# Kernel optimization log

Measured on AMD Instinct MI355X. Metric: run time of the kernel, lower is better.

Reference implementation:

```python
import jax, jax.numpy as jnp
import numpy as np

IN_DIM = 32
OUT_DIM = 32
VAR_DIM = 64
BATCH = 16384
KER_DIMS = [1024, 1024, 1024, 1024]
NUM_STEPS = 8  # fixed-step RK4 stand-in for adaptive odeint (tol=1e-4)


def setup_inputs() -> dict:
    key = jax.random.key(0)
    ks = jax.random.split(key, 12)
    x = jax.random.normal(ks[0], (BATCH, IN_DIM), dtype=jnp.float32)
    aug = jnp.ones((BATCH, VAR_DIM - IN_DIM), dtype=jnp.float32)
    dims = [VAR_DIM] + KER_DIMS + [VAR_DIM]
    inp = {"x": x, "aug": aug}
    for i, (d1, d2) in enumerate(zip(dims[:-1], dims[1:])):
        # Linear(d1+1, d2): weight (d2, d1+1), bias (d2,)
        inp[f"W{i}"] = jax.random.normal(ks[1 + 2 * i], (d2, d1 + 1), dtype=jnp.float32) * 0.02
        inp[f"b{i}"] = jax.random.normal(ks[2 + 2 * i], (d2,), dtype=jnp.float32) * 0.02
    return inp


def _odefunc(t, y, Ws, bs):
    # y: [B, VAR_DIM]; per-layer concat of scalar time column, Linear, ReLU (except last)
    out = y
    n = len(Ws)
    for i, (W, b) in enumerate(zip(Ws, bs)):
        z = jnp.concatenate([out, jnp.full((out.shape[0], 1), t, dtype=out.dtype)], axis=1)
        out = z @ W.T + b
        if i < n - 1:
            out = jax.nn.relu(out)
    return out


def _integrate(y0, Ws, bs):
    dt = jnp.float32(1.0 / NUM_STEPS)

    def rk4_step(y, t):
        k1 = _odefunc(t, y, Ws, bs)
        k2 = _odefunc(t + 0.5 * dt, y + 0.5 * dt * k1, Ws, bs)
        k3 = _odefunc(t + 0.5 * dt, y + 0.5 * dt * k2, Ws, bs)
        k4 = _odefunc(t + dt, y + dt * k3, Ws, bs)
        return y + (dt / 6.0) * (k1 + 2.0 * k2 + 2.0 * k3 + k4), None

    ts = jnp.arange(NUM_STEPS, dtype=jnp.float32) * dt
    y1, _ = jax.lax.scan(rk4_step, y0, ts)
    return y1


def reference(x, aug, W0, b0, W1, b1, W2, b2, W3, b3, W4, b4):
    Ws = (W0, W1, W2, W3, W4)
    bs = (b0, b1, b2, b3, b4)
    y0 = jnp.concatenate([x, aug], axis=1)  # [B, VAR_DIM]
    y1 = _integrate(y0, Ws, bs)
    return y1[:, :OUT_DIM]
```

## Files before the change

kernel.cpp:

```cpp
#include <hip/hip_runtime.h>
#include <cstdint>
#include <cstddef>

#define BATCH 16384

typedef float f32x4 __attribute__((ext_vector_type(4)));
typedef _Float16 f16x8 __attribute__((ext_vector_type(8)));

__device__ __forceinline__ unsigned short f2h_bits(float f) {
  _Float16 h = (_Float16)f;
  return __builtin_bit_cast(unsigned short, h);
}

__device__ __forceinline__ void async_cp16(const void* g, void* l) {
  __builtin_amdgcn_global_load_lds(
      (const __attribute__((address_space(1))) unsigned int*)g,
      (__attribute__((address_space(3))) unsigned int*)l, 16, 0, 0);
}

template <int BM, int BN, int RT, int CT, int K, int N, bool RELU>
__launch_bounds__(256, 2)
__global__ void gemm_h(const unsigned short* __restrict__ A,
                       const unsigned short* __restrict__ Bw,
                       const float* __restrict__ Wfull,
                       const float* __restrict__ bias,
                       float tval,
                       unsigned short* __restrict__ Ch) {
  constexpr int BK = 32;
  constexpr int NI = K / BK;
  __shared__ __align__(16) unsigned short smA[2][BM * BK];
  __shared__ __align__(16) unsigned short smB[2][BN * BK];
  __shared__ float biasLds[BN];

  const int tid = threadIdx.x;
  const int wave = tid >> 6;
  const int lane = tid & 63;
  const int quad = lane >> 4;
  const int r16 = lane & 15;

  const int rowA0 = blockIdx.x * BM;
  const int rowB0 = blockIdx.y * BN;
  const int waveM = wave >> 1;
  const int waveN = wave & 1;

  if (tid < BN) {
    const int col = rowB0 + tid;
    biasLds[tid] = bias[col] + tval * Wfull[(size_t)col * (K + 1) + K];
  }

  auto stage = [&](int k0, int buf) {
#pragma unroll
    for (int i = 0; i < BM * 4 / 256; ++i) {
      const int s = i * 256 + tid;
      const int row = s >> 2;
      const int c = (s & 3) ^ ((row >> 1) & 3);
      const unsigned short* g = A + (size_t)(rowA0 + row) * K + (k0 + c * 8);
      char* l = ((char*)smA[buf]) + (size_t)(i * 256 + (wave << 6)) * 16;
      async_cp16(g, l);
    }
#pragma unroll
    for (int i = 0; i < BN * 4 / 256; ++i) {
      const int s = i * 256 + tid;
      const int row = s >> 2;
      const int c = (s & 3) ^ ((row >> 1) & 3);
      const unsigned short* g = Bw + (size_t)(rowB0 + row) * K + (k0 + c * 8);
      char* l = ((char*)smB[buf]) + (size_t)(i * 256 + (wave << 6)) * 16;
      async_cp16(g, l);
    }
  };

  f32x4 acc[RT][CT];
  const f32x4 zero = {0.f, 0.f, 0.f, 0.f};
#pragma unroll
  for (int i = 0; i < RT; ++i)
#pragma unroll
    for (int j = 0; j < CT; ++j) acc[i][j] = zero;

  stage(0, 0);

#pragma unroll 2
  for (int kk = 0; kk < NI; ++kk) {
    __syncthreads();
    if (kk + 1 < NI) stage((kk + 1) * BK, (kk + 1) & 1);

    const unsigned short* sA = smA[kk & 1];
    const unsigned short* sB = smB[kk & 1];
    f16x8 af[RT], bfr[CT];
#pragma unroll
    for (int nt = 0; nt < CT; ++nt) {
      const int row = (waveN * CT + nt) * 16 + r16;
      const int cp = quad ^ ((row >> 1) & 3);
      bfr[nt] = *(const f16x8*)(sB + row * BK + cp * 8);
    }
#pragma unroll
    for (int mt = 0; mt < RT; ++mt) {
      const int row = (waveM * RT + mt) * 16 + r16;
      const int cp = quad ^ ((row >> 1) & 3);
      af[mt] = *(const f16x8*)(sA + row * BK + cp * 8);
    }
#pragma unroll
    for (int mt = 0; mt < RT; ++mt)
#pragma unroll
      for (int nt = 0; nt < CT; ++nt)
        acc[mt][nt] =
            __builtin_amdgcn_mfma_f32_16x16x32_f16(af[mt], bfr[nt], acc[mt][nt], 0, 0, 0);
  }

#pragma unroll
  for (int mt = 0; mt < RT; ++mt) {
    const int grow0 = rowA0 + (waveM * RT + mt) * 16 + quad * 4;
#pragma unroll
    for (int nt = 0; nt < CT; ++nt) {
      const int lcol = (waveN * CT + nt) * 16 + r16;
      const int gcol = rowB0 + lcol;
      const float bi = biasLds[lcol];
#pragma unroll
      for (int r = 0; r < 4; ++r) {
        float v = acc[mt][nt][r] + bi;
        if (RELU) v = fmaxf(v, 0.0f);
        Ch[(size_t)(grow0 + r) * N + gcol] = f2h_bits(v);
      }
    }
  }
}

__launch_bounds__(256, 4)
__global__ void gemm_l4(const unsigned short* __restrict__ A,
                        const unsigned short* __restrict__ Bw,
                        const float* __restrict__ Wfull,
                        const float* __restrict__ bias,
                        float tval,
                        float* __restrict__ y, float* __restrict__ ksum,
                        unsigned short* __restrict__ yh,
                        float* __restrict__ outp, int mode, float dt) {
  constexpr int K = 1024, BK = 32, BM = 32, BN = 64, NI = K / BK;
  __shared__ __align__(16) unsigned short smA[2][BM * BK];
  __shared__ __align__(16) unsigned short smB[2][BN * BK];
  __shared__ float biasLds[BN];

  const int tid = threadIdx.x;
  const int wave = tid >> 6;
  const int lane = tid & 63;
  const int quad = lane >> 4;
  const int r16 = lane & 15;

  const int rowA0 = blockIdx.x * BM;
  const int waveM = wave >> 1;
  const int waveN = wave & 1;

  if (tid < BN) {
    biasLds[tid] = bias[tid] + tval * Wfull[(size_t)tid * (K + 1) + K];
  }

  auto stage = [&](int k0, int buf) {
    if (tid < BM * 4) {
      const int s = tid;
      const int row = s >> 2;
      const int c = (s & 3) ^ ((row >> 1) & 3);
      const unsigned short* g = A + (size_t)(rowA0 + row) * K + (k0 + c * 8);
      char* l = ((char*)smA[buf]) + (size_t)(wave << 6) * 16;
      async_cp16(g, l);
    }
    {
      const int s = tid;
      const int row = s >> 2;
      const int c = (s & 3) ^ ((row >> 1) & 3);
      const unsigned short* g = Bw + (size_t)row * K + (k0 + c * 8);
      char* l = ((char*)smB[buf]) + (size_t)(wave << 6) * 16;
      async_cp16(g, l);
    }
  };

  f32x4 acc[2];
  const f32x4 zero = {0.f, 0.f, 0.f, 0.f};
  acc[0] = zero; acc[1] = zero;

  stage(0, 0);

#pragma unroll 2
  for (int kk = 0; kk < NI; ++kk) {
    __syncthreads();
    if (kk + 1 < NI) stage((kk + 1) * BK, (kk + 1) & 1);

    const unsigned short* sA = smA[kk & 1];
    const unsigned short* sB = smB[kk & 1];
    f16x8 af, bfr[2];
    {
      const int row = waveM * 16 + r16;
      const int cp = quad ^ ((row >> 1) & 3);
      af = *(const f16x8*)(sA + row * BK + cp * 8);
    }
#pragma unroll
    for (int nt = 0; nt < 2; ++nt) {
      const int row = (waveN * 2 + nt) * 16 + r16;
      const int cp = quad ^ ((row >> 1) & 3);
      bfr[nt] = *(const f16x8*)(sB + row * BK + cp * 8);
    }
#pragma unroll
    for (int nt = 0; nt < 2; ++nt)
      acc[nt] = __builtin_amdgcn_mfma_f32_16x16x32_f16(af, bfr[nt], acc[nt], 0, 0, 0);
  }

  const int grow0 = rowA0 + waveM * 16 + quad * 4;
#pragma unroll
  for (int nt = 0; nt < 2; ++nt) {
    const int col = waveN * 32 + nt * 16 + r16;
    const float bi = biasLds[col];
#pragma unroll
    for (int r = 0; r < 4; ++r) {
      const float k = acc[nt][r] + bi;
      const int row = grow0 + r;
      const int idx = row * 64 + col;
      if (mode == 0) {
        ksum[idx] = k;
        yh[idx] = f2h_bits(y[idx] + 0.5f * dt * k);
      } else if (mode == 1) {
        ksum[idx] += 2.f * k;
        yh[idx] = f2h_bits(y[idx] + 0.5f * dt * k);
      } else if (mode == 2) {
        ksum[idx] += 2.f * k;
        yh[idx] = f2h_bits(y[idx] + dt * k);
      } else {
        const float yn = y[idx] + (dt / 6.f) * (ksum[idx] + k);
        y[idx] = yn;
        yh[idx] = f2h_bits(yn);
        if (outp && col < 32) outp[row * 32 + col] = yn;
      }
    }
  }
}

__global__ void conv_w(const float* __restrict__ W, unsigned short* __restrict__ Wh,
                       int N, int K) {
  const int idx = blockIdx.x * 256 + threadIdx.x;
  if (idx < N * K) {
    const int n = idx / K;
    const int k = idx - n * K;
    Wh[idx] = f2h_bits(W[(size_t)n * (K + 1) + k]);
  }
}

__global__ void init_y(const float* __restrict__ x, const float* __restrict__ aug,
                       float* __restrict__ y, unsigned short* __restrict__ yh) {
  const int idx = blockIdx.x * 256 + threadIdx.x;
  const int i = idx >> 6;
  const int j = idx & 63;
  const float v = (j < 32) ? x[i * 32 + j] : aug[i * 32 + (j - 32)];
  y[idx] = v;
  yh[idx] = f2h_bits(v);
}

extern "C" void kernel_launch(void* const* d_in, const int* in_sizes, int n_in,
                              void* d_out, int out_size, void* d_ws, size_t ws_size,
                              hipStream_t stream) {
  const float* x = (const float*)d_in[0];
  const float* aug = (const float*)d_in[1];
  const float* W[5];
  const float* b[5];
  for (int i = 0; i < 5; ++i) {
    W[i] = (const float*)d_in[2 + 2 * i];
    b[i] = (const float*)d_in[3 + 2 * i];
  }

  char* ws = (char*)d_ws;
  auto alloc = [&](size_t bytes) -> char* {
    char* p = ws;
    ws += (bytes + 255) & ~(size_t)255;
    return p;
  };
  float* y = (float*)alloc((size_t)BATCH * 64 * 4);
  unsigned short* yh = (unsigned short*)alloc((size_t)BATCH * 64 * 2);
  unsigned short* h1 = (unsigned short*)alloc((size_t)BATCH * 1024 * 2);
  unsigned short* h2 = (unsigned short*)alloc((size_t)BATCH * 1024 * 2);
  float* ksum = (float*)alloc((size_t)BATCH * 64 * 4);
  const int Kdim[5] = {64, 1024, 1024, 1024, 1024};
  const int Ndim[5] = {1024, 1024, 1024, 1024, 64};
  unsigned short* Wh[5];
  for (int i = 0; i < 5; ++i)
    Wh[i] = (unsigned short*)alloc((size_t)Ndim[i] * Kdim[i] * 2);

  for (int i = 0; i < 5; ++i) {
    const int total = Ndim[i] * Kdim[i];
    conv_w<<<(total + 255) / 256, 256, 0, stream>>>(W[i], Wh[i], Ndim[i], Kdim[i]);
  }
  init_y<<<BATCH * 64 / 256, 256, 0, stream>>>(x, aug, y, yh);

  const float dt = 0.125f;
  float* outp = (float*)d_out;

  auto eval = [&](float t, int mode, float* op) {
    gemm_h<256, 128, 8, 4, 64, 1024, true>
        <<<dim3(BATCH / 256, 1024 / 128), 256, 0, stream>>>(
            yh, Wh[0], W[0], b[0], t, h1);
    unsigned short* src = h1;
    unsigned short* dst = h2;
    for (int L = 1; L <= 3; ++L) {
      gemm_h<256, 128, 8, 4, 1024, 1024, true>
          <<<dim3(BATCH / 256, 1024 / 128), 256, 0, stream>>>(
              src, Wh[L], W[L], b[L], t, dst);
      unsigned short* tmp = src; src = dst; dst = tmp;
    }
    gemm_l4<<<dim3(BATCH / 32, 1), 256, 0, stream>>>(
        src, Wh[4], W[4], b[4], t, y, ksum, yh, op, mode, dt);
  };

  for (int s = 0; s < 8; ++s) {
    const float t0 = s * dt;
    eval(t0, 0, nullptr);
    eval(t0 + 0.5f * dt, 1, nullptr);
    eval(t0 + 0.5f * dt, 2, nullptr);
    eval(t0 + dt, 3, (s == 7) ? outp : nullptr);
  }
}
```

Baseline: 4.855 ms.

## Pre-tile activations and weights into MFMA fragment layout, load fragments directly from global

Stores weights, activations and the y state in a 16-row tiled layout that matches the MFMA fragment order. Each wave can then load its A/B fragments straight from global memory into registers with register double-buffering, and the LDS staging and per-iteration barriers go away. Epilogues write through an LDS tile so the tiled output is stored as coalesced 16-byte chunks. The trade-offs are the loss of LDS-based reuse across waves, since each wave now reads the B tiles itself and leans on L2, and higher register pressure from full unrolling.

```diff
diff --git a/kernel.cpp b/kernel.cpp
--- a/kernel.cpp
+++ b/kernel.cpp
@@ -12,24 +12,18 @@
   return __builtin_bit_cast(unsigned short, h);
 }
 
-__device__ __forceinline__ void async_cp16(const void* g, void* l) {
-  __builtin_amdgcn_global_load_lds(
-      (const __attribute__((address_space(1))) unsigned int*)g,
-      (__attribute__((address_space(3))) unsigned int*)l, 16, 0, 0);
-}
-
-template <int BM, int BN, int RT, int CT, int K, int N, bool RELU>
+
+template <int RT, int CT, int K, bool RELU>
 __launch_bounds__(256, 2)
 __global__ void gemm_h(const unsigned short* __restrict__ A,
                        const unsigned short* __restrict__ Bw,
                        const float* __restrict__ Wfull,
                        const float* __restrict__ bias,
                        float tval,
-                       unsigned short* __restrict__ Ch) {
-  constexpr int BK = 32;
-  constexpr int NI = K / BK;
-  __shared__ __align__(16) unsigned short smA[2][BM * BK];
-  __shared__ __align__(16) unsigned short smB[2][BN * BK];
+                       unsigned short* __restrict__ Co) {
+  constexpr int NI = K / 32;
+  constexpr int BN = CT * 16;
+  __shared__ unsigned short ctile[256 * 136];
   __shared__ float biasLds[BN];
 
   const int tid = threadIdx.x;
@@ -38,36 +32,22 @@
   const int quad = lane >> 4;
   const int r16 = lane & 15;
 
-  const int rowA0 = blockIdx.x * BM;
+  const int rowA0 = blockIdx.x * 256;
   const int rowB0 = blockIdx.y * BN;
-  const int waveM = wave >> 1;
-  const int waveN = wave & 1;
 
   if (tid < BN) {
     const int col = rowB0 + tid;
     biasLds[tid] = bias[col] + tval * Wfull[(size_t)col * (K + 1) + K];
   }
 
-  auto stage = [&](int k0, int buf) {
-#pragma unroll
-    for (int i = 0; i < BM * 4 / 256; ++i) {
-      const int s = i * 256 + tid;
-      const int row = s >> 2;
-      const int c = (s & 3) ^ ((row >> 1) & 3);
-      const unsigned short* g = A + (size_t)(rowA0 + row) * K + (k0 + c * 8);
-      char* l = ((char*)smA[buf]) + (size_t)(i * 256 + (wave << 6)) * 16;
-      async_cp16(g, l);
-    }
-#pragma unroll
-    for (int i = 0; i < BN * 4 / 256; ++i) {
-      const int s = i * 256 + tid;
-      const int row = s >> 2;
-      const int c = (s & 3) ^ ((row >> 1) & 3);
-      const unsigned short* g = Bw + (size_t)(rowB0 + row) * K + (k0 + c * 8);
-      char* l = ((char*)smB[buf]) + (size_t)(i * 256 + (wave << 6)) * 16;
-      async_cp16(g, l);
-    }
-  };
+  const unsigned short* aptr[RT];
+#pragma unroll
+  for (int mt = 0; mt < RT; ++mt)
+    aptr[mt] = A + (size_t)(rowA0 / 16 + wave * RT + mt) * (K * 16) + lane * 8;
+  const unsigned short* bptr[CT];
+#pragma unroll
+  for (int nt = 0; nt < CT; ++nt)
+    bptr[nt] = Bw + (size_t)(rowB0 / 16 + nt) * (K * 16) + lane * 8;
 
   f32x4 acc[RT][CT];
   const f32x4 zero = {0.f, 0.f, 0.f, 0.f};
@@ -76,55 +56,61 @@
 #pragma unroll
     for (int j = 0; j < CT; ++j) acc[i][j] = zero;
 
-  stage(0, 0);
-
-#pragma unroll 2
+  f16x8 af[2][RT], bf[2][CT];
+  auto loadfr = [&](int kk, int s) {
+#pragma unroll
+    for (int mt = 0; mt < RT; ++mt)
+      af[s][mt] = *(const f16x8*)(aptr[mt] + (size_t)kk * 512);
+#pragma unroll
+    for (int nt = 0; nt < CT; ++nt)
+      bf[s][nt] = *(const f16x8*)(bptr[nt] + (size_t)kk * 512);
+  };
+
+  loadfr(0, 0);
+#pragma unroll
   for (int kk = 0; kk < NI; ++kk) {
-    __syncthreads();
-    if (kk + 1 < NI) stage((kk + 1) * BK, (kk + 1) & 1);
-
-    const unsigned short* sA = smA[kk & 1];
-    const unsigned short* sB = smB[kk & 1];
-    f16x8 af[RT], bfr[CT];
+    const int cur = kk & 1;
+    if (kk + 1 < NI) loadfr(kk + 1, cur ^ 1);
+#pragma unroll
+    for (int mt = 0; mt < RT; ++mt)
+#pragma unroll
+      for (int nt = 0; nt < CT; ++nt)
+        acc[mt][nt] = __builtin_amdgcn_mfma_f32_16x16x32_f16(
+            af[cur][mt], bf[cur][nt], acc[mt][nt], 0, 0, 0);
+  }
+
+  __syncthreads();
+
+#pragma unroll
+  for (int mt = 0; mt < RT; ++mt) {
+    const int row0 = wave * (RT * 16) + mt * 16 + quad * 4;
 #pragma unroll
     for (int nt = 0; nt < CT; ++nt) {
-      const int row = (waveN * CT + nt) * 16 + r16;
-      const int cp = quad ^ ((row >> 1) & 3);
-      bfr[nt] = *(const f16x8*)(sB + row * BK + cp * 8);
-    }
-#pragma unroll
-    for (int mt = 0; mt < RT; ++mt) {
-      const int row = (waveM * RT + mt) * 16 + r16;
-      const int cp = quad ^ ((row >> 1) & 3);
-      af[mt] = *(const f16x8*)(sA + row * BK + cp * 8);
-    }
-#pragma unroll
-    for (int mt = 0; mt < RT; ++mt)
-#pragma unroll
-      for (int nt = 0; nt < CT; ++nt)
-        acc[mt][nt] =
-            __builtin_amdgcn_mfma_f32_16x16x32_f16(af[mt], bfr[nt], acc[mt][nt], 0, 0, 0);
-  }
-
-#pragma unroll
-  for (int mt = 0; mt < RT; ++mt) {
-    const int grow0 = rowA0 + (waveM * RT + mt) * 16 + quad * 4;
-#pragma unroll
-    for (int nt = 0; nt < CT; ++nt) {
-      const int lcol = (waveN * CT + nt) * 16 + r16;
-      const int gcol = rowB0 + lcol;
-      const float bi = biasLds[lcol];
+      const int col = nt * 16 + r16;
+      const float bi = biasLds[col];
 #pragma unroll
       for (int r = 0; r < 4; ++r) {
         float v = acc[mt][nt][r] + bi;
         if (RELU) v = fmaxf(v, 0.0f);
-        Ch[(size_t)(grow0 + r) * N + gcol] = f2h_bits(v);
+        ctile[(row0 + r) * 136 + col] = f2h_bits(v);
       }
     }
   }
-}
-
-__launch_bounds__(256, 4)
+  __syncthreads();
+
+#pragma unroll
+  for (int i = 0; i < 16; ++i) {
+    const int chunk = i * 256 + tid;
+    const int r = chunk & 15;
+    const int kc = (chunk >> 4) & 15;
+    const int mt2 = chunk >> 8;
+    f16x8 vv = *(const f16x8*)(ctile + (mt2 * 16 + r) * 136 + kc * 8);
+    *(f16x8*)(Co + ((size_t)(rowA0 / 16 + mt2) * 128 + (rowB0 / 8 + kc)) * 128 +
+              r * 8) = vv;
+  }
+}
+
+__launch_bounds__(256, 2)
 __global__ void gemm_l4(const unsigned short* __restrict__ A,
                         const unsigned short* __restrict__ Bw,
                         const float* __restrict__ Wfull,
@@ -133,10 +119,9 @@
                         float* __restrict__ y, float* __restrict__ ksum,
                         unsigned short* __restrict__ yh,
                         float* __restrict__ outp, int mode, float dt) {
-  constexpr int K = 1024, BK = 32, BM = 32, BN = 64, NI = K / BK;
-  __shared__ __align__(16) unsigned short smA[2][BM * BK];
-  __shared__ __align__(16) unsigned short smB[2][BN * BK];
-  __shared__ float biasLds[BN];
+  constexpr int K = 1024, NI = K / 32;
+  __shared__ unsigned short ytile[32 * 72];
+  __shared__ float biasLds[64];
 
   const int tid = threadIdx.x;
   const int wave = tid >> 6;
@@ -144,64 +129,47 @@
   const int quad = lane >> 4;
   const int r16 = lane & 15;
 
-  const int rowA0 = blockIdx.x * BM;
+  const int rowA0 = blockIdx.x * 32;
   const int waveM = wave >> 1;
   const int waveN = wave & 1;
 
-  if (tid < BN) {
+  if (tid < 64) {
     biasLds[tid] = bias[tid] + tval * Wfull[(size_t)tid * (K + 1) + K];
   }
 
-  auto stage = [&](int k0, int buf) {
-    if (tid < BM * 4) {
-      const int s = tid;
-      const int row = s >> 2;
-      const int c = (s & 3) ^ ((row >> 1) & 3);
-      const unsigned short* g = A + (size_t)(rowA0 + row) * K + (k0 + c * 8);
-      char* l = ((char*)smA[buf]) + (size_t)(wave << 6) * 16;
-      async_cp16(g, l);
-    }
-    {
-      const int s = tid;
-      const int row = s >> 2;
-      const int c = (s & 3) ^ ((row >> 1) & 3);
-      const unsigned short* g = Bw + (size_t)row * K + (k0 + c * 8);
-      char* l = ((char*)smB[buf]) + (size_t)(wave << 6) * 16;
-      async_cp16(g, l);
-    }
-  };
+  const unsigned short* aptr =
+      A + (size_t)(rowA0 / 16 + waveM) * (K * 16) + lane * 8;
+  const unsigned short* bptr[2];
+#pragma unroll
+  for (int nt = 0; nt < 2; ++nt)
+    bptr[nt] = Bw + (size_t)(waveN * 2 + nt) * (K * 16) + lane * 8;
 
   f32x4 acc[2];
   const f32x4 zero = {0.f, 0.f, 0.f, 0.f};
   acc[0] = zero; acc[1] = zero;
 
-  stage(0, 0);
-
-#pragma unroll 2
+  f16x8 af[2], bf[2][2];
+  auto loadfr = [&](int kk, int s) {
+    af[s] = *(const f16x8*)(aptr + (size_t)kk * 512);
+#pragma unroll
+    for (int nt = 0; nt < 2; ++nt)
+      bf[s][nt] = *(const f16x8*)(bptr[nt] + (size_t)kk * 512);
+  };
+
+  loadfr(0, 0);
+#pragma unroll
   for (int kk = 0; kk < NI; ++kk) {
-    __syncthreads();
-    if (kk + 1 < NI) stage((kk + 1) * BK, (kk + 1) & 1);
-
-    const unsigned short* sA = smA[kk & 1];
-    const unsigned short* sB = smB[kk & 1];
-    f16x8 af, bfr[2];
-    {
-      const int row = waveM * 16 + r16;
-      const int cp = quad ^ ((row >> 1) & 3);
-      af = *(const f16x8*)(sA + row * BK + cp * 8);
-    }
-#pragma unroll
-    for (int nt = 0; nt < 2; ++nt) {
-      const int row = (waveN * 2 + nt) * 16 + r16;
-      const int cp = quad ^ ((row >> 1) & 3);
-      bfr[nt] = *(const f16x8*)(sB + row * BK + cp * 8);
-    }
+    const int cur = kk & 1;
+    if (kk + 1 < NI) loadfr(kk + 1, cur ^ 1);
 #pragma unroll
     for (int nt = 0; nt < 2; ++nt)
-      acc[nt] = __builtin_amdgcn_mfma_f32_16x16x32_f16(af, bfr[nt], acc[nt], 0, 0, 0);
-  }
-
-  const int grow0 = rowA0 + waveM * 16 + quad * 4;
+      acc[nt] = __builtin_amdgcn_mfma_f32_16x16x32_f16(af[cur], bf[cur][nt],
+                                                       acc[nt], 0, 0, 0);
+  }
+
+  __syncthreads();
+
+  const int lrow0 = waveM * 16 + quad * 4;
 #pragma unroll
   for (int nt = 0; nt < 2; ++nt) {
     const int col = waveN * 32 + nt * 16 + r16;
@@ -209,45 +177,62 @@
 #pragma unroll
     for (int r = 0; r < 4; ++r) {
       const float k = acc[nt][r] + bi;
-      const int row = grow0 + r;
-      const int idx = row * 64 + col;
+      const int grow = rowA0 + lrow0 + r;
+      const int idx = grow * 64 + col;
+      const float yv = y[idx];
+      float ynext;
       if (mode == 0) {
         ksum[idx] = k;
-        yh[idx] = f2h_bits(y[idx] + 0.5f * dt * k);
+        ynext = yv + 0.5f * dt * k;
       } else if (mode == 1) {
         ksum[idx] += 2.f * k;
-        yh[idx] = f2h_bits(y[idx] + 0.5f * dt * k);
+        ynext = yv + 0.5f * dt * k;
       } else if (mode == 2) {
         ksum[idx] += 2.f * k;
-        yh[idx] = f2h_bits(y[idx] + dt * k);
+        ynext = yv + dt * k;
       } else {
-        const float yn = y[idx] + (dt / 6.f) * (ksum[idx] + k);
-        y[idx] = yn;
-        yh[idx] = f2h_bits(yn);
-        if (outp && col < 32) outp[row * 32 + col] = yn;
+        ynext = yv + (dt / 6.f) * (ksum[idx] + k);
+        y[idx] = ynext;
+        if (outp && col < 32) outp[grow * 32 + col] = ynext;
       }
+      ytile[(lrow0 + r) * 72 + col] = f2h_bits(ynext);
     }
+  }
+  __syncthreads();
+
+  {
+    const int r = tid & 15;
+    const int kc = (tid >> 4) & 7;
+    const int mt2 = tid >> 7;
+    f16x8 vv = *(const f16x8*)(ytile + (mt2 * 16 + r) * 72 + kc * 8);
+    *(f16x8*)(yh + ((size_t)(rowA0 / 16 + mt2) * 8 + kc) * 128 + r * 8) = vv;
   }
 }
 
 __global__ void conv_w(const float* __restrict__ W, unsigned short* __restrict__ Wh,
                        int N, int K) {
   const int idx = blockIdx.x * 256 + threadIdx.x;
-  if (idx < N * K) {
-    const int n = idx / K;
-    const int k = idx - n * K;
-    Wh[idx] = f2h_bits(W[(size_t)n * (K + 1) + k]);
-  }
+  if (idx >= N * K) return;
+  const int c = idx & 7;
+  const int r = (idx >> 3) & 15;
+  const int blk = idx >> 7;
+  const int kc = blk % (K / 8);
+  const int ntile = blk / (K / 8);
+  Wh[idx] = f2h_bits(W[(size_t)(ntile * 16 + r) * (K + 1) + kc * 8 + c]);
 }
 
 __global__ void init_y(const float* __restrict__ x, const float* __restrict__ aug,
                        float* __restrict__ y, unsigned short* __restrict__ yh) {
   const int idx = blockIdx.x * 256 + threadIdx.x;
-  const int i = idx >> 6;
-  const int j = idx & 63;
+  const int c = idx & 7;
+  const int r = (idx >> 3) & 15;
+  const int kc = (idx >> 7) & 7;
+  const int mtile = idx >> 10;
+  const int i = mtile * 16 + r;
+  const int j = kc * 8 + c;
   const float v = (j < 32) ? x[i * 32 + j] : aug[i * 32 + (j - 32)];
-  y[idx] = v;
   yh[idx] = f2h_bits(v);
+  y[i * 64 + j] = v;
 }
 
 extern "C" void kernel_launch(void* const* d_in, const int* in_sizes, int n_in,
@@ -289,13 +274,13 @@
   float* outp = (float*)d_out;
 
   auto eval = [&](float t, int mode, float* op) {
-    gemm_h<256, 128, 8, 4, 64, 1024, true>
+    gemm_h<4, 8, 64, true>
         <<<dim3(BATCH / 256, 1024 / 128), 256, 0, stream>>>(
             yh, Wh[0], W[0], b[0], t, h1);
     unsigned short* src = h1;
     unsigned short* dst = h2;
     for (int L = 1; L <= 3; ++L) {
-      gemm_h<256, 128, 8, 4, 1024, 1024, true>
+      gemm_h<4, 8, 1024, true>
           <<<dim3(BATCH / 256, 1024 / 128), 256, 0, stream>>>(
               src, Wh[L], W[L], b[L], t, dst);
       unsigned short* tmp = src; src = dst; dst = tmp;
```

Result: slower. 10.46 ms (+115.5%).
